# Optimization experiments

Hardware: AMD Instinct MI355X
Metric: run time of the kernel (lower is better)

## Reference

```python
import jax, jax.numpy as jnp
import numpy as np

B, E, S, W, M, C, O = 2048, 16, 512, 512, 64, 64, 8

def hardsigmoid(x):
    return jnp.clip((x + 3.0) / 6.0, 0.0, 1.0)

def swish(x):
    return x * jax.nn.sigmoid(x)

def setup_inputs() -> dict:
    key = jax.random.key(0)
    ks = jax.random.split(key, 16)
    scale = 1.0  # 1/(in_channels*out_channels) with in=out=1
    d = {}
    d["x"] = jax.random.normal(ks[0], (B, E * S), jnp.float32)
    d["codes"] = jax.random.normal(ks[1], (E, C), jnp.float32) * 0.1
    d["p_w"] = jax.random.normal(ks[2], (2 * W, 2 * S), jnp.float32) * 0.02
    d["p_b"] = jnp.zeros((2 * W,), jnp.float32)
    d["com0"] = jax.random.uniform(ks[3], (M, 2), jnp.float32) * scale
    d["code0"] = jax.random.uniform(ks[4], (C, M, 2), jnp.float32) * scale
    d["filt0"] = -3.0 * jnp.ones((M,), jnp.float32)
    d["com1"] = jax.random.uniform(ks[5], (M, 2), jnp.float32) * scale
    d["code1"] = jax.random.uniform(ks[6], (C, M, 2), jnp.float32) * scale
    d["filt1"] = -3.0 * jnp.ones((M,), jnp.float32)
    d["w0_w"] = jax.random.normal(ks[7], (2 * W, 2 * W), jnp.float32) * 0.02
    d["w0_b"] = jnp.zeros((2 * W,), jnp.float32)
    d["w1_w"] = jax.random.normal(ks[8], (2 * W, 2 * W), jnp.float32) * 0.02
    d["w1_b"] = jnp.zeros((2 * W,), jnp.float32)
    # fc1: Conv1d(2W -> (O//2)*W, k=1, groups=W): per group 2 in -> O//2 out
    d["fc1_w"] = jax.random.normal(ks[9], (W, O // 2, 2), jnp.float32) * 0.1
    d["fc1_b"] = jnp.zeros((W * (O // 2),), jnp.float32)
    d["fc2_w"] = jax.random.normal(ks[10], (O, W * (O // 2)), jnp.float32) * 0.02
    d["fc2_b"] = jnp.zeros((O,), jnp.float32)
    return d

def spectral(x3, codes, com, codew, filt):
    # x3: [B, E, L] with in_channels=out_channels=1; L = 2*W
    L = x3.shape[-1]
    m = filt.shape[0]
    xf = jnp.fft.rfft(x3, axis=-1)                      # [B, E, L//2+1] complex64
    lam = hardsigmoid(filt)                              # [m]
    com_c = com[:, 0] + 1j * com[:, 1]                   # [m]
    env = jnp.einsum('ec,cmk->emk', codes, codew)        # [E, m, 2]
    env_c = env[..., 0] + 1j * env[..., 1]               # [E, m]
    xm = xf[:, :, :m]                                    # [B, E, m]
    out_m = lam * xm * com_c + (1.0 - lam) * xm * env_c[None]
    out_f = jnp.zeros_like(xf).at[:, :, :m].set(out_m)
    return jnp.fft.irfft(out_f, n=L, axis=-1)            # [B, E, L]

def reference(x, codes, p_w, p_b, com0, code0, filt0, com1, code1, filt1,
              w0_w, w0_b, w1_w, w1_b, fc1_w, fc1_b, fc2_w, fc2_b):
    bsz = x.shape[0]
    e = codes.shape[0]
    s = x.shape[1] // e
    xv = x.reshape(bsz, e, s)
    grid = jnp.broadcast_to(jnp.linspace(0.0, 1.0, s, dtype=x.dtype), (bsz, e, s))
    h = jnp.concatenate([xv, grid], axis=-1).reshape(bsz * e, 2 * s)
    h = h @ p_w.T + p_b                                  # [BE, 2W]
    twoW = h.shape[-1]
    h3 = h.reshape(bsz, e, twoW)
    x1 = spectral(h3, codes, com0, code0, filt0)
    x2 = h @ w0_w.T + w0_b
    h3 = swish(x1 + x2.reshape(bsz, e, twoW))
    h = h3.reshape(bsz * e, twoW)
    x1 = spectral(h3, codes, com1, code1, filt1)
    x2 = h @ w1_w.T + w1_b
    h = (x1 + x2.reshape(bsz, e, twoW)).reshape(bsz * e, twoW)
    # grouped pointwise fc1: groups = W, 2 in-ch per group -> O//2 out-ch per group
    wd = fc1_w.shape[0]
    hg = h.reshape(bsz * e, wd, 2)
    h = jnp.einsum('ngk,gok->ngo', hg, fc1_w).reshape(bsz * e, -1) + fc1_b
    h = swish(h)
    h = h @ fc2_w.T + fc2_b                              # [BE, O]
    return h.reshape(bsz, -1)                            # [B, E*O]
```

## Files before the change

### kernel.cpp

```cpp
#include <hip/hip_runtime.h>
#include <hip/hip_bf16.h>
#include <cstdint>


typedef __bf16 bf16;
typedef __attribute__((ext_vector_type(8))) __bf16 bf16x8;
typedef __attribute__((ext_vector_type(4))) __bf16 bf16x4;
typedef __attribute__((ext_vector_type(4))) float f32x4;

#define N_ROWS 32768

__device__ __forceinline__ void gl_lds16(const void* g, void* l) {
    __builtin_amdgcn_global_load_lds(
        (const __attribute__((address_space(1))) void*)g,
        (__attribute__((address_space(3))) void*)l,
        16, 0, 0);
}

__device__ __forceinline__ float swishf(float v) {
    return v / (1.f + __expf(-v));
}


__global__ __launch_bounds__(256) void build_cmix(const float* __restrict__ codes,
                                                  const float* __restrict__ com,
                                                  const float* __restrict__ code,
                                                  const float* __restrict__ filt,
                                                  float2* __restrict__ cmix) {
    int t = blockIdx.x * 256 + threadIdx.x;
    if (t >= 16 * 64) return;
    int e = t >> 6, m = t & 63;
    float er = 0.f, ei = 0.f;
    for (int c = 0; c < 64; ++c) {
        float cd = codes[e * 64 + c];
        er += cd * code[(c * 64 + m) * 2 + 0];
        ei += cd * code[(c * 64 + m) * 2 + 1];
    }
    float f = filt[m];
    float lam = fminf(fmaxf((f + 3.f) * (1.f / 6.f), 0.f), 1.f);
    float cr = lam * com[m * 2 + 0] + (1.f - lam) * er;
    float ci = lam * com[m * 2 + 1] + (1.f - lam) * ei;
    float g = (m == 0) ? (1.f / 1024.f) : (2.f / 1024.f);
    cmix[t] = make_float2(g * cr, g * ci);
}

__global__ __launch_bounds__(256) void build_fb2(float* __restrict__ Fb32,
                                                 bf16* __restrict__ Fbb) {
    int t = blockIdx.x * 256 + threadIdx.x;
    int rr = t >> 10, s = t & 1023;
    int k = rr >> 1;
    int ph = (k * s) & 1023;
    float ang = (float)ph * 6.1359231515425649e-3f;
    float v = (rr & 1) ? -sinf(ang) : cosf(ang);
    Fb32[t] = v;
    Fbb[t] = (bf16)v;
}

__global__ __launch_bounds__(256) void build_bcat(const float* __restrict__ w,
                                                  bf16* __restrict__ out) {
    int t = blockIdx.x * 256 + threadIdx.x;
    if (t >= 1024 * 1152) return;
    int j = t / 1152, c = t % 1152;
    float v;
    if (c < 1024) {
        v = w[j * 1024 + c];
    } else {
        int cc = c - 1024, k = cc >> 1;
        int ph = (k * j) & 1023;
        float ang = (float)ph * 6.1359231515425649e-3f;
        v = (cc & 1) ? -sinf(ang) : cosf(ang);
    }
    out[t] = (bf16)v;
}

__global__ __launch_bounds__(256) void build_g(const float* __restrict__ Fb32,
                                               const float* __restrict__ p_w,
                                               float* __restrict__ G32) {
    int c = blockIdx.x * 256 + threadIdx.x;
    int k2 = blockIdx.y;
    const float* fb = Fb32 + k2 * 1024;
    float a = 0.f;
    #pragma unroll 8
    for (int w = 0; w < 1024; ++w)
        a += fb[w] * p_w[(size_t)w * 1024 + c];
    G32[k2 * 512 + c] = a;
}

__global__ __launch_bounds__(256) void build_bias1a(const float* __restrict__ p_w,
                                                    const float* __restrict__ p_b,
                                                    float* __restrict__ bias1) {
    int w = (blockIdx.x * 256 + threadIdx.x) >> 6;
    int lane = threadIdx.x & 63;
    const float* src = p_w + (size_t)w * 1024 + 512 + lane * 8;
    float4 v0 = *(const float4*)(src);
    float4 v1 = *(const float4*)(src + 4);
    float s0 = (float)(lane * 8) * (1.f / 511.f);
    const float st = 1.f / 511.f;
    float a = v0.x * s0 + v0.y * (s0 + st) + v0.z * (s0 + 2 * st) + v0.w * (s0 + 3 * st)
            + v1.x * (s0 + 4 * st) + v1.y * (s0 + 5 * st) + v1.z * (s0 + 6 * st) + v1.w * (s0 + 7 * st);
    #pragma unroll
    for (int msk = 1; msk < 64; msk <<= 1) a += __shfl_xor(a, msk);
    if (lane == 0) bias1[w] = p_b[w] + a;
}

__global__ __launch_bounds__(256) void build_bias1b(const float* __restrict__ Fb32,
                                                    float* __restrict__ bias1) {
    int k2 = blockIdx.x * 4 + (threadIdx.x >> 6);
    int lane = threadIdx.x & 63;
    const float* fb = Fb32 + (size_t)k2 * 1024 + lane * 16;
    const float* bb = bias1 + lane * 16;
    float a = 0.f;
    #pragma unroll
    for (int j = 0; j < 4; ++j) {
        float4 f = *(const float4*)(fb + 4 * j);
        float4 b = *(const float4*)(bb + 4 * j);
        a += f.x * b.x + f.y * b.y + f.z * b.z + f.w * b.w;
    }
    #pragma unroll
    for (int msk = 1; msk < 64; msk <<= 1) a += __shfl_xor(a, msk);
    if (lane == 0) {
        bias1[1024 + k2] = a;
        bias1[1152 + k2] = 0.f;
    }
}

__global__ __launch_bounds__(256) void build_wp(const float* __restrict__ p_w,
                                                const float* __restrict__ G32,
                                                bf16* __restrict__ WP) {
    int t = blockIdx.x * 256 + threadIdx.x;
    if (t >= 1280 * 512) return;
    int r = t >> 9, c = t & 511;
    float v = (r < 1024) ? p_w[(size_t)r * 1024 + c]
            : (r < 1152) ? G32[(r - 1024) * 512 + c] : 0.f;
    WP[t] = (bf16)v;
}

__global__ __launch_bounds__(256) void convert_x(const float* __restrict__ x,
                                                 bf16* __restrict__ A0) {
    int t = blockIdx.x * 256 + threadIdx.x;
    const float4* xp = (const float4*)(x + (size_t)t * 8);
    float4 a = xp[0], b = xp[1];
    bf16x8 o;
    o[0] = (bf16)a.x; o[1] = (bf16)a.y; o[2] = (bf16)a.z; o[3] = (bf16)a.w;
    o[4] = (bf16)b.x; o[5] = (bf16)b.y; o[6] = (bf16)b.z; o[7] = (bf16)b.w;
    *(bf16x8*)(A0 + (size_t)t * 8) = o;
}

template<int ACT, int HASMIX>
__global__ __launch_bounds__(512, 2)
void gemm256(const bf16* __restrict__ A, int lda,
             const bf16* __restrict__ Bt, int ldb,
             const float* __restrict__ bias,
             bf16* __restrict__ Cout, int ldc,
             const float2* __restrict__ cmix, int ncols,
             int K, int NX, int NY) {
    __shared__ bf16 sA[2][256 * 64];
    __shared__ bf16 sB[2][256 * 64];
    const int tid = threadIdx.x;
    const int wave = tid >> 6, lane = tid & 63;
    const int wm = wave >> 2, wn = wave & 3;

    int tx, ty;
    if ((NX & 7) == 0) {
        int xcd = blockIdx.x & 7;
        int pos = blockIdx.x >> 3;
        ty = pos % NY;
        tx = (pos / NY) * 8 + xcd;
    } else {
        tx = blockIdx.x % NX;
        ty = blockIdx.x / NX;
    }
    const int rowA0 = tx * 256;
    const int rowB0 = ty * 256;

    f32x4 acc[8][4];
    #pragma unroll
    for (int m = 0; m < 8; ++m)
        #pragma unroll
        for (int n = 0; n < 4; ++n)
            acc[m][n] = f32x4{0.f, 0.f, 0.f, 0.f};

    const int srq = lane >> 3;
    const int ssl = (lane & 7) ^ srq;
    const bf16* gA = A + (size_t)(rowA0 + wave * 8 + srq) * lda + ssl * 8;
    const bf16* gB = Bt + (size_t)(rowB0 + wave * 8 + srq) * ldb + ssl * 8;

    const int NT = K / 64;
    auto STAGE = [&](int t) {
        const int slot = t & 1;
        const size_t ko = (size_t)t * 64;
        #pragma unroll
        for (int j = 0; j < 4; ++j) {
            gl_lds16(gA + (size_t)j * 64 * lda + ko, &sA[slot][(j * 64 + wave * 8) * 64]);
            gl_lds16(gB + (size_t)j * 64 * ldb + ko, &sB[slot][(j * 64 + wave * 8) * 64]);
        }
    };

    STAGE(0);

    const int p = lane & 15, q = lane >> 4;
    const int axr = (p & 7) << 4;

    for (int t = 0; t < NT; ++t) {
        asm volatile("s_waitcnt vmcnt(0)" ::: "memory");
        __builtin_amdgcn_s_barrier();
        __builtin_amdgcn_sched_barrier(0);
        if (t + 1 < NT) STAGE(t + 1);
        const char* sa = (const char*)sA[t & 1];
        const char* sb = (const char*)sB[t & 1];
        #pragma unroll
        for (int kk = 0; kk < 64; kk += 32) {
            bf16x8 af[8], bfr[4];
            #pragma unroll
            for (int m = 0; m < 8; ++m) {
                int off = (((wm * 128 + m * 16 + p) * 64 + kk + q * 8) * 2) ^ axr;
                af[m] = *(const bf16x8*)(sa + off);
            }
            #pragma unroll
            for (int n = 0; n < 4; ++n) {
                int off = (((wn * 64 + n * 16 + p) * 64 + kk + q * 8) * 2) ^ axr;
                bfr[n] = *(const bf16x8*)(sb + off);
            }
            asm volatile("s_waitcnt lgkmcnt(0)" ::: "memory");
            __builtin_amdgcn_sched_barrier(0);
            __builtin_amdgcn_s_setprio(1);
            #pragma unroll
            for (int m = 0; m < 8; ++m)
                #pragma unroll
                for (int n = 0; n < 4; ++n)
                    acc[m][n] = __builtin_amdgcn_mfma_f32_16x16x32_bf16(af[m], bfr[n], acc[m][n], 0, 0, 0);
            __builtin_amdgcn_s_setprio(0);
            __builtin_amdgcn_sched_barrier(0);
        }
    }

    const int rowb = rowA0 + wm * 128;
    const int colb = rowB0 + wn * 64;
    #pragma unroll
    for (int m = 0; m < 8; ++m) {
        #pragma unroll
        for (int n = 0; n < 4; ++n) {
            int col = colb + n * 16 + p;
            float bv = bias ? bias[col] : 0.f;
            #pragma unroll
            for (int r = 0; r < 4; ++r) {
                int row = rowb + m * 16 + q * 4 + r;
                float v = acc[m][n][r] + bv;
                if (HASMIX) {
                    float pp = __shfl_xor(v, 1);
                    if (col >= 1024) {
                        int k = (col - 1024) >> 1;
                        float2 c = cmix[(row & 15) * 64 + k];
                        v = v * c.x + (((p & 1) == 0) ? -pp * c.y : pp * c.y);
                    }
                    if (col < ncols) Cout[(size_t)row * ldc + col] = (bf16)v;
                } else {
                    if (ACT) v = swishf(v);
                    Cout[(size_t)row * ldc + col] = (bf16)v;
                }
            }
        }
    }
}

__global__ __launch_bounds__(256)
void gemm_mix(const bf16* __restrict__ A, int lda,
              const bf16* __restrict__ Bt, int ldb,
              void* __restrict__ Cout, int ldc,
              const float2* __restrict__ cmix,
              int K) {
    __shared__ bf16 sA[128 * 64];
    __shared__ bf16 sB[128 * 64];
    const int tid = threadIdx.x;
    const int wave = tid >> 6;
    const int lane = tid & 63;
    const int wm = wave >> 1, wn = wave & 1;
    const int rowA0 = blockIdx.x * 128;

    f32x4 acc[4][4];
    #pragma unroll
    for (int m = 0; m < 4; ++m)
        #pragma unroll
        for (int n = 0; n < 4; ++n)
            acc[m][n] = f32x4{0.f, 0.f, 0.f, 0.f};

    const int srow = wave * 32 + (lane >> 3);
    const int scol = (lane & 7) * 8;
    const bf16* gA = A + (size_t)(rowA0 + srow) * lda + scol;
    const bf16* gB = Bt + (size_t)srow * ldb + scol;
    bf16* lA = &sA[(wave * 32) * 64];
    bf16* lB = &sB[(wave * 32) * 64];

    for (int k0 = 0; k0 < K; k0 += 64) {
        __syncthreads();
        #pragma unroll
        for (int i = 0; i < 4; ++i) {
            gl_lds16(gA + (size_t)i * 8 * lda + k0, lA + i * 8 * 64);
            gl_lds16(gB + (size_t)i * 8 * ldb + k0, lB + i * 8 * 64);
        }
        __syncthreads();
        #pragma unroll
        for (int kk = 0; kk < 64; kk += 32) {
            bf16x8 af[4], bfr[4];
            #pragma unroll
            for (int m = 0; m < 4; ++m)
                af[m] = *(const bf16x8*)&sA[(wm * 64 + m * 16 + (lane & 15)) * 64 + kk + ((lane >> 4) * 8)];
            #pragma unroll
            for (int n = 0; n < 4; ++n)
                bfr[n] = *(const bf16x8*)&sB[(wn * 64 + n * 16 + (lane & 15)) * 64 + kk + ((lane >> 4) * 8)];
            #pragma unroll
            for (int m = 0; m < 4; ++m)
                #pragma unroll
                for (int n = 0; n < 4; ++n)
                    acc[m][n] = __builtin_amdgcn_mfma_f32_16x16x32_bf16(af[m], bfr[n], acc[m][n], 0, 0, 0);
        }
    }

    const int rowb = rowA0 + wm * 64;
    #pragma unroll
    for (int m = 0; m < 4; ++m) {
        #pragma unroll
        for (int n = 0; n < 4; ++n) {
            int col = wn * 64 + n * 16 + (lane & 15);
            int k = col >> 1;
            #pragma unroll
            for (int r = 0; r < 4; ++r) {
                float v = acc[m][n][r];
                float pp = __shfl_xor(v, 1);
                int row = rowb + m * 16 + (lane >> 4) * 4 + r;
                float2 c = cmix[(row & 15) * 64 + k];
                float val = v * c.x + (((lane & 1) == 0) ? -pp * c.y : pp * c.y);
                ((bf16*)Cout)[(size_t)row * ldc + col] = (bf16)val;
            }
        }
    }
}

__global__ __launch_bounds__(256) void fc_fused(const bf16* __restrict__ H,
                                                const float* __restrict__ w1,
                                                const float* __restrict__ b1,
                                                const float* __restrict__ w2,
                                                const float* __restrict__ b2,
                                                float* __restrict__ out) {
    __shared__ bf16 sw2[8][2048];
    __shared__ bf16 ss[2048];
    int tid = threadIdx.x;
    for (int i = tid * 4; i < 8 * 2048; i += 1024) {
        float4 v = *(const float4*)(w2 + i);
        bf16x4 b = {(bf16)v.x, (bf16)v.y, (bf16)v.z, (bf16)v.w};
        *(bf16x4*)&sw2[0][i] = b;
    }

    float wv[16];
    const float4* w1p = (const float4*)(w1 + tid * 16);
    *(float4*)&wv[0]  = w1p[0];
    *(float4*)&wv[4]  = w1p[1];
    *(float4*)&wv[8]  = w1p[2];
    *(float4*)&wv[12] = w1p[3];
    float bb[8];
    const float4* b1p = (const float4*)(b1 + tid * 8);
    *(float4*)&bb[0] = b1p[0];
    *(float4*)&bb[4] = b1p[1];
    __syncthreads();

    for (int r = 0; r < 16; ++r) {
        int n = blockIdx.x * 16 + r;
        bf16x4 hv = *(const bf16x4*)(H + (size_t)n * 1024 + tid * 4);
        float hh[4] = {(float)hv[0], (float)hv[1], (float)hv[2], (float)hv[3]};
        bf16x8 sb;
        #pragma unroll
        for (int jj = 0; jj < 8; ++jj) {
            float h0 = hh[(jj >> 2) * 2];
            float h1 = hh[(jj >> 2) * 2 + 1];
            float t = h0 * wv[2 * jj] + h1 * wv[2 * jj + 1] + bb[jj];
            sb[jj] = (bf16)swishf(t);
        }
        *(bf16x8*)&ss[tid * 8] = sb;
        __syncthreads();
        int o8 = tid >> 5, l5 = tid & 31;
        float p = 0.f;
        #pragma unroll
        for (int i = 0; i < 16; ++i) {
            bf16x4 a = *(const bf16x4*)&ss[4 * l5 + 128 * i];
            bf16x4 b = *(const bf16x4*)&sw2[o8][4 * l5 + 128 * i];
            p += (float)a[0] * (float)b[0] + (float)a[1] * (float)b[1]
               + (float)a[2] * (float)b[2] + (float)a[3] * (float)b[3];
        }
        #pragma unroll
        for (int msk = 1; msk < 32; msk <<= 1) p += __shfl_xor(p, msk);
        if (l5 == 0) out[(size_t)n * 8 + o8] = p + b2[o8];
        __syncthreads();
    }
}


extern "C" void kernel_launch(void* const* d_in, const int* in_sizes, int n_in,
                              void* d_out, int out_size, void* d_ws, size_t ws_size,
                              hipStream_t stream) {
    const float* x     = (const float*)d_in[0];
    const float* codes = (const float*)d_in[1];
    const float* p_w   = (const float*)d_in[2];
    const float* p_b   = (const float*)d_in[3];
    const float* com0  = (const float*)d_in[4];
    const float* code0 = (const float*)d_in[5];
    const float* filt0 = (const float*)d_in[6];
    const float* com1  = (const float*)d_in[7];
    const float* code1 = (const float*)d_in[8];
    const float* filt1 = (const float*)d_in[9];
    const float* w0_w  = (const float*)d_in[10];
    const float* w0_b  = (const float*)d_in[11];
    const float* w1_w  = (const float*)d_in[12];
    const float* w1_b  = (const float*)d_in[13];
    const float* fc1w  = (const float*)d_in[14];
    const float* fc1b  = (const float*)d_in[15];
    const float* fc2w  = (const float*)d_in[16];
    const float* fc2b  = (const float*)d_in[17];
    float* out = (float*)d_out;

    char* ws = (char*)d_ws;
    bf16*  WP   = (bf16*)(ws + 0);
    bf16*  B0   = (bf16*)(ws + 1310720);
    bf16*  B1   = (bf16*)(ws + 3670016);
    bf16*  Fbb  = (bf16*)(ws + 6029312);
    float* Fb32 = (float*)(ws + 6291456);
    float* G32  = (float*)(ws + 6815744);
    float* bias1= (float*)(ws + 7077888);
    float2* cm0 = (float2*)(ws + 7083008);
    float2* cm1 = (float2*)(ws + 7091200);
    const size_t CB = 7099392;

    const size_t PER_ROW = 2048 + 2304 + 2304;
    long rmax = 0;
    if (ws_size > CB) rmax = (long)((ws_size - CB) / PER_ROW) / 256 * 256;
    if (rmax > N_ROWS) rmax = N_ROWS;
    if (rmax < 256) {
        hipMemsetAsync(d_out, 0, (size_t)out_size * sizeof(float), stream);
        return;
    }
    const int R = (int)rmax;

    build_cmix<<<4, 256, 0, stream>>>(codes, com0, code0, filt0, cm0);
    build_cmix<<<4, 256, 0, stream>>>(codes, com1, code1, filt1, cm1);
    build_fb2<<<512, 256, 0, stream>>>(Fb32, Fbb);
    build_bcat<<<4608, 256, 0, stream>>>(w0_w, B0);
    build_bcat<<<4608, 256, 0, stream>>>(w1_w, B1);
    build_g<<<dim3(2, 128), 256, 0, stream>>>(Fb32, p_w, G32);
    build_bias1a<<<256, 256, 0, stream>>>(p_w, p_b, bias1);
    build_bias1b<<<32, 256, 0, stream>>>(Fb32, bias1);
    build_wp<<<2560, 256, 0, stream>>>(p_w, G32, WP);

    char* cb = ws + CB;
    for (int row0 = 0; row0 < N_ROWS; row0 += R) {
        const int r = (N_ROWS - row0 < R) ? (N_ROWS - row0) : R;
        bf16*  A0  = (bf16*)cb;
        bf16*  H3b = (bf16*)cb;
        bf16*  A1  = (bf16*)(cb + (size_t)R * 2048);
        bf16*  A2  = (bf16*)(cb + (size_t)R * 2048 + (size_t)R * 2304);
        const int NX = r / 256;

        convert_x<<<r / 4, 256, 0, stream>>>(x + (size_t)row0 * 512, A0);

        gemm256<0, 1><<<NX * 5, 512, 0, stream>>>(
            A0, 512, WP, 512, bias1, A1, 1152, cm0, 1152, 512, NX, 5);
        gemm256<1, 0><<<NX * 4, 512, 0, stream>>>(
            A1, 1152, B0, 1152, w0_b, A2, 1152, nullptr, 1024, 1152, NX, 4);
        gemm_mix<<<dim3(r / 128, 1), 256, 0, stream>>>(
            A2, 1152, Fbb, 1024, (void*)(A2 + 1024), 1152, cm1, 1024);
        gemm256<0, 0><<<NX * 4, 512, 0, stream>>>(
            A2, 1152, B1, 1152, w1_b, H3b, 1024, nullptr, 1024, 1152, NX, 4);
        fc_fused<<<r / 16, 256, 0, stream>>>(H3b, fc1w, fc1b, fc2w, fc2b, out + (size_t)row0 * 8);
    }
}
```

Before: 512.4 us.

## Fuse final GEMM with grouped fc1, swish and fc2 into one kernel

The last layer GEMM and the separate fc_fused kernel are replaced by a single gemm_fc kernel. It computes 128 rows against all 1024 columns in four column passes, then applies bias, grouped fc1, swish and the fc2 reduction in registers via shuffles, accumulating into shared memory. This removes the bf16 H3b round trip through global memory and one launch, and shrinks the per-row workspace. In exchange each block does four sequential N-tiles and uses large LDS and register footprints, with fewer blocks (r/128), which may reduce occupancy and parallelism.

```diff
diff --git a/kernel.cpp b/kernel.cpp
--- a/kernel.cpp
+++ b/kernel.cpp
@@ -263,6 +263,151 @@
     }
 }
 
+__global__ __launch_bounds__(512, 2)
+void gemm_fc(const bf16* __restrict__ A, int lda,
+             const bf16* __restrict__ Bt, int ldb,
+             const float* __restrict__ hbias,
+             const float* __restrict__ w1,
+             const float* __restrict__ b1,
+             const float* __restrict__ w2,
+             const float* __restrict__ b2,
+             float* __restrict__ out,
+             int K) {
+    __shared__ bf16 sA[2][128 * 64];
+    __shared__ bf16 sB[2][256 * 64];
+    __shared__ float outacc[4][128][8];
+    const int tid = threadIdx.x;
+    const int wave = tid >> 6, lane = tid & 63;
+    const int wm = wave >> 2, wn = wave & 3;
+    const int rowA0 = blockIdx.x * 128;
+
+    for (int i = tid; i < 4 * 128 * 8; i += 512) ((float*)outacc)[i] = 0.f;
+    __syncthreads();
+
+    const int srq = lane >> 3;
+    const int ssl = (lane & 7) ^ srq;
+    const bf16* gA = A + (size_t)(rowA0 + wave * 8 + srq) * lda + ssl * 8;
+    const int p = lane & 15, q = lane >> 4;
+    const int axr = (p & 7) << 4;
+    const int pe = p & 1;
+    const int NT = K / 64;
+
+    for (int nt = 0; nt < 4; ++nt) {
+        const bf16* gB = Bt + (size_t)(nt * 256 + wave * 8 + srq) * ldb + ssl * 8;
+
+        f32x4 acc[4][4];
+        #pragma unroll
+        for (int m = 0; m < 4; ++m)
+            #pragma unroll
+            for (int n = 0; n < 4; ++n)
+                acc[m][n] = f32x4{0.f, 0.f, 0.f, 0.f};
+
+        auto STAGE = [&](int t) {
+            const int slot = t & 1;
+            const size_t ko = (size_t)t * 64;
+            #pragma unroll
+            for (int j = 0; j < 2; ++j)
+                gl_lds16(gA + (size_t)j * 64 * lda + ko, &sA[slot][(j * 64 + wave * 8) * 64]);
+            #pragma unroll
+            for (int j = 0; j < 4; ++j)
+                gl_lds16(gB + (size_t)j * 64 * ldb + ko, &sB[slot][(j * 64 + wave * 8) * 64]);
+        };
+
+        STAGE(0);
+        for (int t = 0; t < NT; ++t) {
+            asm volatile("s_waitcnt vmcnt(0)" ::: "memory");
+            __builtin_amdgcn_s_barrier();
+            __builtin_amdgcn_sched_barrier(0);
+            if (t + 1 < NT) STAGE(t + 1);
+            const char* sa = (const char*)sA[t & 1];
+            const char* sb = (const char*)sB[t & 1];
+            #pragma unroll
+            for (int kk = 0; kk < 64; kk += 32) {
+                bf16x8 af[4], bfr[4];
+                #pragma unroll
+                for (int m = 0; m < 4; ++m)
+                    af[m] = *(const bf16x8*)(sa + ((((wm * 64 + m * 16 + p) * 64 + kk + q * 8) * 2) ^ axr));
+                #pragma unroll
+                for (int n = 0; n < 4; ++n)
+                    bfr[n] = *(const bf16x8*)(sb + ((((wn * 64 + n * 16 + p) * 64 + kk + q * 8) * 2) ^ axr));
+                asm volatile("s_waitcnt lgkmcnt(0)" ::: "memory");
+                __builtin_amdgcn_sched_barrier(0);
+                __builtin_amdgcn_s_setprio(1);
+                #pragma unroll
+                for (int m = 0; m < 4; ++m)
+                    #pragma unroll
+                    for (int n = 0; n < 4; ++n)
+                        acc[m][n] = __builtin_amdgcn_mfma_f32_16x16x32_bf16(af[m], bfr[n], acc[m][n], 0, 0, 0);
+                __builtin_amdgcn_s_setprio(0);
+                __builtin_amdgcn_sched_barrier(0);
+            }
+        }
+
+        float hb[4], w1o0[4][2], w1o1[4][2], fb0[4], fb1[4];
+        float f2a[4][8], f2b[4][8];
+        #pragma unroll
+        for (int n = 0; n < 4; ++n) {
+            int col = nt * 256 + wn * 64 + n * 16 + p;
+            int g = col >> 1;
+            int o0 = pe * 2, o1 = pe * 2 + 1;
+            hb[n] = hbias[col];
+            w1o0[n][0] = w1[g * 8 + o0 * 2 + 0];
+            w1o0[n][1] = w1[g * 8 + o0 * 2 + 1];
+            w1o1[n][0] = w1[g * 8 + o1 * 2 + 0];
+            w1o1[n][1] = w1[g * 8 + o1 * 2 + 1];
+            fb0[n] = b1[g * 4 + o0];
+            fb1[n] = b1[g * 4 + o1];
+            #pragma unroll
+            for (int o8 = 0; o8 < 8; ++o8) {
+                f2a[n][o8] = w2[o8 * 2048 + g * 4 + o0];
+                f2b[n][o8] = w2[o8 * 2048 + g * 4 + o1];
+            }
+        }
+        #pragma unroll
+        for (int m = 0; m < 4; ++m) {
+            #pragma unroll
+            for (int r = 0; r < 4; ++r) {
+                float part[8];
+                #pragma unroll
+                for (int o8 = 0; o8 < 8; ++o8) part[o8] = 0.f;
+                #pragma unroll
+                for (int n = 0; n < 4; ++n) {
+                    float v = acc[m][n][r] + hb[n];
+                    float vp = __shfl_xor(v, 1);
+                    float ve = pe ? vp : v;
+                    float vo = pe ? v : vp;
+                    float s0 = swishf(ve * w1o0[n][0] + vo * w1o0[n][1] + fb0[n]);
+                    float s1 = swishf(ve * w1o1[n][0] + vo * w1o1[n][1] + fb1[n]);
+                    #pragma unroll
+                    for (int o8 = 0; o8 < 8; ++o8)
+                        part[o8] += s0 * f2a[n][o8] + s1 * f2b[n][o8];
+                }
+                #pragma unroll
+                for (int msk = 1; msk < 16; msk <<= 1)
+                    #pragma unroll
+                    for (int o8 = 0; o8 < 8; ++o8)
+                        part[o8] += __shfl_xor(part[o8], msk);
+                if (p == 0) {
+                    int lrow = wm * 64 + m * 16 + q * 4 + r;
+                    #pragma unroll
+                    for (int o8 = 0; o8 < 8; ++o8)
+                        outacc[wn][lrow][o8] += part[o8];
+                }
+            }
+        }
+    }
+
+    __syncthreads();
+    #pragma unroll
+    for (int ii = 0; ii < 2; ++ii) {
+        int idx = tid + ii * 512;
+        int lrow = idx >> 3, o8 = idx & 7;
+        float v = outacc[0][lrow][o8] + outacc[1][lrow][o8]
+                + outacc[2][lrow][o8] + outacc[3][lrow][o8] + b2[o8];
+        out[(size_t)(rowA0 + lrow) * 8 + o8] = v;
+    }
+}
+
 __global__ __launch_bounds__(256)
 void gemm_mix(const bf16* __restrict__ A, int lda,
               const bf16* __restrict__ Bt, int ldb,
@@ -333,63 +478,6 @@
                 ((bf16*)Cout)[(size_t)row * ldc + col] = (bf16)val;
             }
         }
-    }
-}
-
-__global__ __launch_bounds__(256) void fc_fused(const bf16* __restrict__ H,
-                                                const float* __restrict__ w1,
-                                                const float* __restrict__ b1,
-                                                const float* __restrict__ w2,
-                                                const float* __restrict__ b2,
-                                                float* __restrict__ out) {
-    __shared__ bf16 sw2[8][2048];
-    __shared__ bf16 ss[2048];
-    int tid = threadIdx.x;
-    for (int i = tid * 4; i < 8 * 2048; i += 1024) {
-        float4 v = *(const float4*)(w2 + i);
-        bf16x4 b = {(bf16)v.x, (bf16)v.y, (bf16)v.z, (bf16)v.w};
-        *(bf16x4*)&sw2[0][i] = b;
-    }
-
-    float wv[16];
-    const float4* w1p = (const float4*)(w1 + tid * 16);
-    *(float4*)&wv[0]  = w1p[0];
-    *(float4*)&wv[4]  = w1p[1];
-    *(float4*)&wv[8]  = w1p[2];
-    *(float4*)&wv[12] = w1p[3];
-    float bb[8];
-    const float4* b1p = (const float4*)(b1 + tid * 8);
-    *(float4*)&bb[0] = b1p[0];
-    *(float4*)&bb[4] = b1p[1];
-    __syncthreads();
-
-    for (int r = 0; r < 16; ++r) {
-        int n = blockIdx.x * 16 + r;
-        bf16x4 hv = *(const bf16x4*)(H + (size_t)n * 1024 + tid * 4);
-        float hh[4] = {(float)hv[0], (float)hv[1], (float)hv[2], (float)hv[3]};
-        bf16x8 sb;
-        #pragma unroll
-        for (int jj = 0; jj < 8; ++jj) {
-            float h0 = hh[(jj >> 2) * 2];
-            float h1 = hh[(jj >> 2) * 2 + 1];
-            float t = h0 * wv[2 * jj] + h1 * wv[2 * jj + 1] + bb[jj];
-            sb[jj] = (bf16)swishf(t);
-        }
-        *(bf16x8*)&ss[tid * 8] = sb;
-        __syncthreads();
-        int o8 = tid >> 5, l5 = tid & 31;
-        float p = 0.f;
-        #pragma unroll
-        for (int i = 0; i < 16; ++i) {
-            bf16x4 a = *(const bf16x4*)&ss[4 * l5 + 128 * i];
-            bf16x4 b = *(const bf16x4*)&sw2[o8][4 * l5 + 128 * i];
-            p += (float)a[0] * (float)b[0] + (float)a[1] * (float)b[1]
-               + (float)a[2] * (float)b[2] + (float)a[3] * (float)b[3];
-        }
-        #pragma unroll
-        for (int msk = 1; msk < 32; msk <<= 1) p += __shfl_xor(p, msk);
-        if (l5 == 0) out[(size_t)n * 8 + o8] = p + b2[o8];
-        __syncthreads();
     }
 }
 
@@ -429,7 +517,7 @@
     float2* cm1 = (float2*)(ws + 7091200);
     const size_t CB = 7099392;
 
-    const size_t PER_ROW = 2048 + 2304 + 2304;
+    const size_t PER_ROW = 1024 + 2304 + 2304;
     long rmax = 0;
     if (ws_size > CB) rmax = (long)((ws_size - CB) / PER_ROW) / 256 * 256;
     if (rmax > N_ROWS) rmax = N_ROWS;
@@ -453,9 +541,8 @@
     for (int row0 = 0; row0 < N_ROWS; row0 += R) {
         const int r = (N_ROWS - row0 < R) ? (N_ROWS - row0) : R;
         bf16*  A0  = (bf16*)cb;
-        bf16*  H3b = (bf16*)cb;
-        bf16*  A1  = (bf16*)(cb + (size_t)R * 2048);
-        bf16*  A2  = (bf16*)(cb + (size_t)R * 2048 + (size_t)R * 2304);
+        bf16*  A1  = (bf16*)(cb + (size_t)R * 1024);
+        bf16*  A2  = (bf16*)(cb + (size_t)R * 1024 + (size_t)R * 2304);
         const int NX = r / 256;
 
         convert_x<<<r / 4, 256, 0, stream>>>(x + (size_t)row0 * 512, A0);
@@ -466,8 +553,7 @@
             A1, 1152, B0, 1152, w0_b, A2, 1152, nullptr, 1024, 1152, NX, 4);
         gemm_mix<<<dim3(r / 128, 1), 256, 0, stream>>>(
             A2, 1152, Fbb, 1024, (void*)(A2 + 1024), 1152, cm1, 1024);
-        gemm256<0, 0><<<NX * 4, 512, 0, stream>>>(
-            A2, 1152, B1, 1152, w1_b, H3b, 1024, nullptr, 1024, 1152, NX, 4);
-        fc_fused<<<r / 16, 256, 0, stream>>>(H3b, fc1w, fc1b, fc2w, fc2b, out + (size_t)row0 * 8);
-    }
-}
+        gemm_fc<<<r / 128, 512, 0, stream>>>(
+            A2, 1152, B1, 1152, w1_b, fc1w, fc1b, fc2w, fc2b, out + (size_t)row0 * 8, 1152);
+    }
+}
```

After: 513.8 us. No clear change (+0.3%).
